# Optimization experiments

Measured on AMD Instinct MI355X. Metric: run time of the kernel, lower is better.

## Reference

```python
import jax, jax.numpy as jnp
import numpy as np

NEG_SLOPE = 0.2
EPS = 1e-16  # PyG softmax eps


def gat_layer(x, edge_index, W_lin, b_lin, W_attn, b_attn):
    # GATConv: add self loops, x = lin(x), per-edge attention, segment softmax over
    # target nodes (edge_index[1]), scatter-add of x_j * alpha.
    N = x.shape[0]
    loops = jnp.arange(N, dtype=edge_index.dtype)
    src = jnp.concatenate([edge_index[0], loops])  # j (source / neighbor)
    dst = jnp.concatenate([edge_index[1], loops])  # i (target)
    x = x @ W_lin.T + b_lin                        # [N, D]
    D = x.shape[1]
    xi = x[dst]                                    # [E, D]
    xj = x[src]                                    # [E, D]
    # attn(cat(x_i, x_j)) split to avoid materializing the [E, 2D] concat
    Wi, Wj = W_attn[:, :D], W_attn[:, D:]
    alpha = xi @ Wi.T + xj @ Wj.T + b_attn         # [E, D]
    alpha = jax.nn.leaky_relu(alpha, NEG_SLOPE)
    # numerically stable segment softmax grouped by dst (per output channel)
    m = jax.ops.segment_max(alpha, dst, num_segments=N)
    alpha = jnp.exp(alpha - m[dst])
    denom = jax.ops.segment_sum(alpha, dst, num_segments=N)
    alpha = alpha / (denom[dst] + EPS)
    return jax.ops.segment_sum(xj * alpha, dst, num_segments=N)


def setup_inputs() -> dict:
    key = jax.random.key(0)
    ks = jax.random.split(key, 22)
    B, L, NN, E = 64, 50, 500, 256000
    EMB, D = 128, 128
    N = B * NN
    w = lambda k, shape: jax.random.normal(k, shape, jnp.float32) * 0.05
    return {
        "x": jax.random.normal(ks[0], (N, EMB), jnp.float32),
        "edge_index_0": jax.random.randint(ks[1], (2, E), 0, N, jnp.int32),
        "edge_index_1": jax.random.randint(ks[2], (2, E), 0, N, jnp.int32),
        "state_": jax.random.normal(ks[3], (B, D), jnp.float32),
        "input_": jax.random.normal(ks[4], (B, L, EMB), jnp.float32),
        "W_in": w(ks[5], (D, EMB)),
        "W_z": w(ks[6], (D, 2 * D)),
        "W_r": w(ks[7], (D, 2 * D)),
        "W_h": w(ks[8], (D, 2 * D)),
        "g0_Wlin": w(ks[9], (D, EMB)),
        "g0_blin": w(ks[10], (D,)),
        "g0_Wattn": w(ks[11], (D, 2 * D)),
        "g0_battn": w(ks[12], (D,)),
        "g1_Wlin": w(ks[13], (D, D)),
        "g1_blin": w(ks[14], (D,)),
        "g1_Wattn": w(ks[15], (D, 2 * D)),
        "g1_battn": w(ks[16], (D,)),
        "Wp": w(ks[17], (1, D)),
        "bp": w(ks[18], (1,)),
        "Ws": w(ks[19], (1, D)),
        "bs": w(ks[20], (1,)),
    }


def reference(x, edge_index_0, edge_index_1, state_, input_,
              W_in, W_z, W_r, W_h,
              g0_Wlin, g0_blin, g0_Wattn, g0_battn,
              g1_Wlin, g1_blin, g1_Wattn, g1_battn,
              Wp, bp, Ws, bs):
    B, D = state_.shape
    n_nodes = x.shape[0] // B
    # GRU-style gate on global state
    inp = jnp.mean(input_ @ W_in.T, axis=1)                 # [B, D]
    zi = jnp.concatenate([state_, inp], axis=-1)            # [B, 2D]
    z = jax.nn.sigmoid(zi @ W_z.T)
    r = jax.nn.sigmoid(zi @ W_r.T)
    h = jnp.tanh(jnp.concatenate([r * state_, inp], -1) @ W_h.T)
    h = (1 - z) * state_ + z * h                            # [B, D]
    # two GAT layers
    g0 = gat_layer(x, edge_index_0, g0_Wlin, g0_blin, g0_Wattn, g0_battn)
    g1 = gat_layer(g0, edge_index_1, g1_Wlin, g1_blin, g1_Wattn, g1_battn)
    xg = g1.reshape(B, n_nodes, D) * h[:, None, :]          # broadcast gate
    prob = (xg @ Wp.T + bp).reshape(B, n_nodes)
    sisr = jax.nn.sigmoid((xg @ Ws.T + bs).reshape(B, n_nodes))
    prob = jax.nn.softmax(prob[:, 1:], axis=-1)             # drop depot node 0
    return prob, sisr, h
```

## Files before the change

### kernel.cpp

```cpp
#include <hip/hip_runtime.h>
#include <math.h>

#define CAP  32
#define CAPB 4096
#define PART_CHUNK 4096

typedef __attribute__((ext_vector_type(8))) short bfrag;
typedef __attribute__((ext_vector_type(4))) float ffrag;
typedef __attribute__((ext_vector_type(2))) float f2v;

__device__ __forceinline__ float sigmoidf_(float x){ return 1.f/(1.f+__expf(-x)); }

__device__ __forceinline__ unsigned short f2bf(float f){
    unsigned u = __float_as_uint(f);
    u += 0x7fffu + ((u >> 16) & 1u);
    return (unsigned short)(u >> 16);
}
__device__ __forceinline__ float bf2f(unsigned u){
    return __uint_as_float((u & 0xffffu) << 16);
}

__global__ __launch_bounds__(256) void prep_kernel(
    const int* __restrict__ ei0, const int* __restrict__ ei1,
    int* __restrict__ binCnt, unsigned* __restrict__ bins, int E, int nA, int nb,
    const float* __restrict__ state_, const float* __restrict__ input_,
    const float* __restrict__ W_in, const float* __restrict__ W_z,
    const float* __restrict__ W_r, const float* __restrict__ W_h,
    float* __restrict__ h_out, int L,
    const float* __restrict__ Wlin0, const float* __restrict__ Wattn0,
    const float* __restrict__ blin0, const float* __restrict__ battn0,
    const float* __restrict__ Wlin1, const float* __restrict__ Wattn1,
    const float* __restrict__ blin1, const float* __restrict__ battn1,
    unsigned short* __restrict__ wc, float* __restrict__ bc, int B)
{
    int blk = blockIdx.x;
    if (blk < 2 * nA) {
        __shared__ int lcnt[128];
        __shared__ int gbase[128];
        int g = (blk >= nA) ? 1 : 0;
        const int* ei = g ? ei1 : ei0;
        int base = (blk - g * nA) * PART_CHUNK;
        int tid = threadIdx.x;
        for (int t = tid; t < nb; t += 256) lcnt[t] = 0;
        __syncthreads();
        int lpos[16], binv[16]; unsigned wrd[16];
        #pragma unroll
        for (int i = 0; i < 16; ++i) {
            int e = base + i * 256 + tid;
            if (e < E) {
                int d = ei[E + e];
                int s = ei[e];
                int b = d >> 8;
                binv[i] = b;
                wrd[i]  = ((unsigned)(d & 255) << 24) | (unsigned)s;
                lpos[i] = atomicAdd(&lcnt[b], 1);
            } else binv[i] = -1;
        }
        __syncthreads();
        if (tid < nb) gbase[tid] = atomicAdd(&binCnt[g * nb + tid], lcnt[tid]);
        __syncthreads();
        #pragma unroll
        for (int i = 0; i < 16; ++i) {
            if (binv[i] >= 0) {
                int pos = gbase[binv[i]] + lpos[i];
                if (pos < CAPB) bins[(size_t)(g * nb + binv[i]) * CAPB + pos] = wrd[i];
            }
        }
    } else if (blk < 2 * nA + B) {
        __shared__ float mu[128];
        __shared__ float zi[256];
        __shared__ float zi2[256];
        int b = blk - 2 * nA;
        int tid = threadIdx.x;
        float st = 0.f, inp = 0.f, z = 0.f, r = 0.f;
        if (tid < 128) {
            float s = 0.f;
            const float* ip = input_ + (size_t)b * L * 128 + tid;
            for (int l = 0; l < L; ++l) s += ip[(size_t)l * 128];
            mu[tid] = s / (float)L;
        }
        __syncthreads();
        if (tid < 128) {
            const float* wr = W_in + (size_t)tid * 128;
            for (int k = 0; k < 128; ++k) inp += mu[k] * wr[k];
            st = state_[b * 128 + tid];
            zi[tid] = st; zi[128 + tid] = inp;
        }
        __syncthreads();
        if (tid < 128) {
            float az = 0.f, ar = 0.f;
            const float* wz = W_z + (size_t)tid * 256;
            const float* wrr = W_r + (size_t)tid * 256;
            for (int k = 0; k < 256; ++k) { float v = zi[k]; az += v * wz[k]; ar += v * wrr[k]; }
            z = sigmoidf_(az); r = sigmoidf_(ar);
            zi2[tid] = r * st; zi2[128 + tid] = inp;
        }
        __syncthreads();
        if (tid < 128) {
            float ah = 0.f;
            const float* wh = W_h + (size_t)tid * 256;
            for (int k = 0; k < 256; ++k) ah += zi2[k] * wh[k];
            float hc = tanhf(ah);
            h_out[b * 128 + tid] = (1.f - z) * st + z * hc;
        }
    } else {
        int idx = (blk - 2 * nA - B) * 256 + threadIdx.x;
        if (idx < 2 * 384 * 128) {
            int layer = idx / 49152;
            int t = idx - layer * 49152;
            int n = t >> 7, k = t & 127;
            const float* Wlin  = layer ? Wlin1  : Wlin0;
            const float* Wattn = layer ? Wattn1 : Wattn0;
            float v;
            if (n < 128) {
                v = Wlin[n * 128 + k];
            } else {
                int rr = (n < 256) ? (n - 128) : (n - 256);
                int off = (n < 256) ? 0 : 128;
                float s = 0.f;
                for (int d = 0; d < 128; ++d) s += Wattn[rr * 256 + off + d] * Wlin[d * 128 + k];
                v = s;
            }
            wc[idx] = f2bf(v);
        } else if (idx < 2 * 384 * 128 + 768) {
            int bi = idx - 2 * 384 * 128;
            int layer = bi / 384;
            int n = bi - layer * 384;
            const float* blin  = layer ? blin1  : blin0;
            const float* Wattn = layer ? Wattn1 : Wattn0;
            const float* battn = layer ? battn1 : battn0;
            float v;
            if (n < 128) v = blin[n];
            else {
                int rr = (n < 256) ? (n - 128) : (n - 256);
                int off = (n < 256) ? 0 : 128;
                float s = 0.f;
                for (int d = 0; d < 128; ++d) s += Wattn[rr * 256 + off + d] * blin[d];
                v = (n < 256) ? (s + battn[rr]) : s;
            }
            bc[bi] = v;
        }
    }
}

__global__ __launch_bounds__(256) void gemm384(const short* __restrict__ Xb, const float* __restrict__ Xf,
                                               const short* __restrict__ Wc, const float* __restrict__ bc,
                                               unsigned short* __restrict__ aib, unsigned short* __restrict__ pair,
                                               const unsigned* __restrict__ bins, const int* __restrict__ binCnt,
                                               int* __restrict__ cnt, unsigned short* __restrict__ esrc,
                                               int N, int nb, int gemmBlks)
{
    if ((int)blockIdx.x >= gemmBlks) {
        __shared__ int cl[256];
        __shared__ __align__(16) unsigned short el[256 * CAP];
        int p = blockIdx.x - gemmBlks;
        int g = (p >= nb) ? 1 : 0;
        int bin = p - g * nb;
        int tid = threadIdx.x;
        cl[tid] = 0;
        __syncthreads();
        int m = binCnt[g * nb + bin]; if (m > CAPB) m = CAPB;
        const unsigned* bp_ = bins + (size_t)(g * nb + bin) * CAPB;
        for (int i = tid; i < m; i += 256) {
            unsigned w = bp_[i];
            int dl = (int)(w >> 24);
            int pp = atomicAdd(&cl[dl], 1);
            if (pp < CAP) el[dl * CAP + pp] = (unsigned short)w;
        }
        __syncthreads();
        int nodeBase = bin * 256;
        int* cg = cnt + (size_t)g * N;
        if (nodeBase + tid < N) cg[nodeBase + tid] = cl[tid];
        uint4* eo = (uint4*)(esrc + ((size_t)g * N + nodeBase) * CAP);
        const uint4* es = (const uint4*)el;
        #pragma unroll
        for (int k = 0; k < 4; ++k) eo[k * 256 + tid] = es[k * 256 + tid];
        return;
    }
    __shared__ __align__(16) short wlds[384 * 40];
    int tid = threadIdx.x;
    int lane = tid & 63, wave = tid >> 6;
    int quad = lane >> 4, l16 = lane & 15;
    int mrow = blockIdx.x * 64 + wave * 16 + l16;

    bfrag av[4];
    if (Xf) {
        #pragma unroll
        for (int kk = 0; kk < 4; ++kk) {
            const float* xfp = Xf + (size_t)mrow * 128 + quad * 8 + kk * 32;
            float4 a0 = *(const float4*)(xfp);
            float4 a1 = *(const float4*)(xfp + 4);
            av[kk] = (bfrag){ (short)f2bf(a0.x), (short)f2bf(a0.y), (short)f2bf(a0.z), (short)f2bf(a0.w),
                              (short)f2bf(a1.x), (short)f2bf(a1.y), (short)f2bf(a1.z), (short)f2bf(a1.w) };
        }
    } else {
        #pragma unroll
        for (int kk = 0; kk < 4; ++kk)
            av[kk] = *(const bfrag*)(Xb + (size_t)mrow * 128 + quad * 8 + kk * 32);
    }

    ffrag acc[24];
    #pragma unroll
    for (int t = 0; t < 24; ++t) acc[t] = (ffrag){0.f, 0.f, 0.f, 0.f};

    #pragma unroll
    for (int kk = 0; kk < 4; ++kk) {
        __syncthreads();
        #pragma unroll
        for (int it = 0; it < 6; ++it) {
            int slot = it * 256 + tid;
            int row = slot >> 2, ch = slot & 3;
            *(bfrag*)&wlds[row * 40 + ch * 8] = *(const bfrag*)(Wc + (size_t)row * 128 + kk * 32 + ch * 8);
        }
        __syncthreads();
        #pragma unroll
        for (int t = 0; t < 24; ++t) {
            bfrag bv = *(const bfrag*)&wlds[(t * 16 + l16) * 40 + quad * 8];
            acc[t] = __builtin_amdgcn_mfma_f32_16x16x32_bf16(av[kk], bv, acc[t], 0, 0, 0);
        }
    }
    int rbase = blockIdx.x * 64 + wave * 16 + quad * 4;
    #pragma unroll
    for (int t = 0; t < 8; ++t) {
        int c = t * 16 + l16;
        float by = bc[c], bi = bc[128 + c], bj = bc[256 + c];
        #pragma unroll
        for (int r = 0; r < 4; ++r) {
            size_t off = (size_t)(rbase + r) * 128 + c;
            float yv  = acc[t][r]      + by;
            float aiv = acc[8 + t][r]  + bi;
            float ajv = acc[16 + t][r] + bj;
            aib[off] = f2bf(aiv);
            int w = __builtin_amdgcn_cvt_pk_fp8_f32(yv, ajv, 0, false);
            pair[off] = (unsigned short)w;
        }
    }
}

__global__ void aggregate_kernel(const unsigned short* __restrict__ aib, const unsigned* __restrict__ pair,
                                 const int* __restrict__ cnt, const unsigned short* __restrict__ esrc,
                                 unsigned* __restrict__ gb_out,
                                 const float* __restrict__ h, const float* __restrict__ Wp, const float* __restrict__ bp,
                                 const float* __restrict__ Ws, const float* __restrict__ bs,
                                 float* __restrict__ pbuf, float* __restrict__ sisr_out,
                                 int N, int NN, int fuse_score)
{
    int node = blockIdx.x * (blockDim.x >> 6) + (threadIdx.x >> 6);
    if (node >= N) return;
    int lane = threadIdx.x & 63;
    int c = 2 * lane;
    unsigned ain2 = *(const unsigned*)(aib + ((size_t)node << 7) + c);
    float ain0 = bf2f(ain2), ain1 = bf2f(ain2 >> 16);
    int deg = cnt[node]; if (deg > CAP) deg = CAP;
    const unsigned short* ep = esrc + (size_t)node * CAP;
    int myidx = (lane < deg) ? (int)ep[lane] : 0;

    float w0 = 0.f, w1 = 0.f, o0 = 0.f, o1 = 0.f;
    #define PROC(q) { \
        f2v lo = __builtin_amdgcn_cvt_pk_f32_fp8((int)(q), false); \
        f2v hi = __builtin_amdgcn_cvt_pk_f32_fp8((int)(q), true); \
        float a0 = ain0 + lo.y; \
        float a1 = ain1 + hi.y; \
        a0 = (a0 > 0.f) ? a0 : 0.2f * a0; \
        a1 = (a1 > 0.f) ? a1 : 0.2f * a1; \
        float e0 = __expf(a0), e1 = __expf(a1); \
        w0 += e0; w1 += e1; \
        o0 += e0 * lo.x; o1 += e1 * hi.x; }

    unsigned qs = pair[((size_t)node << 6) + lane];
    PROC(qs)

    int j = 0;
    for (; j + 8 <= deg; j += 8) {
        int s0 = __shfl(myidx, j),     s1 = __shfl(myidx, j + 1);
        int s2 = __shfl(myidx, j + 2), s3 = __shfl(myidx, j + 3);
        int s4 = __shfl(myidx, j + 4), s5 = __shfl(myidx, j + 5);
        int s6 = __shfl(myidx, j + 6), s7 = __shfl(myidx, j + 7);
        unsigned q0 = pair[((size_t)s0 << 6) + lane];
        unsigned q1 = pair[((size_t)s1 << 6) + lane];
        unsigned q2 = pair[((size_t)s2 << 6) + lane];
        unsigned q3 = pair[((size_t)s3 << 6) + lane];
        unsigned q4 = pair[((size_t)s4 << 6) + lane];
        unsigned q5 = pair[((size_t)s5 << 6) + lane];
        unsigned q6 = pair[((size_t)s6 << 6) + lane];
        unsigned q7 = pair[((size_t)s7 << 6) + lane];
        PROC(q0) PROC(q1) PROC(q2) PROC(q3) PROC(q4) PROC(q5) PROC(q6) PROC(q7)
    }
    if (j + 4 <= deg) {
        int s0 = __shfl(myidx, j),     s1 = __shfl(myidx, j + 1);
        int s2 = __shfl(myidx, j + 2), s3 = __shfl(myidx, j + 3);
        unsigned q0 = pair[((size_t)s0 << 6) + lane];
        unsigned q1 = pair[((size_t)s1 << 6) + lane];
        unsigned q2 = pair[((size_t)s2 << 6) + lane];
        unsigned q3 = pair[((size_t)s3 << 6) + lane];
        PROC(q0) PROC(q1) PROC(q2) PROC(q3)
        j += 4;
    }
    for (; j < deg; ++j) {
        int s0 = __shfl(myidx, j);
        unsigned q0 = pair[((size_t)s0 << 6) + lane];
        PROC(q0)
    }
    #undef PROC

    float g0 = o0 / (w0 + 1e-16f), g1 = o1 / (w1 + 1e-16f);
    if (!fuse_score) {
        gb_out[(size_t)node * 64 + lane] = (unsigned)f2bf(g0) | ((unsigned)f2bf(g1) << 16);
    } else {
        int b = node / NN;
        float xg0 = g0 * h[b * 128 + c], xg1 = g1 * h[b * 128 + c + 1];
        float pp = xg0 * Wp[c] + xg1 * Wp[c + 1];
        float ss = xg0 * Ws[c] + xg1 * Ws[c + 1];
        #pragma unroll
        for (int o = 32; o > 0; o >>= 1) { pp += __shfl_xor(pp, o); ss += __shfl_xor(ss, o); }
        if (lane == 0) {
            pbuf[node] = pp + bp[0];
            sisr_out[node] = sigmoidf_(ss + bs[0]);
        }
    }
}

__global__ void softmax_kernel(const float* __restrict__ pbuf, float* __restrict__ prob_out, int NN){
    int b = blockIdx.x, tid = threadIdx.x;
    __shared__ float sdata[512];
    bool valid = (tid >= 1 && tid < NN);
    float v = valid ? pbuf[b * NN + tid] : -INFINITY;
    sdata[tid] = v; __syncthreads();
    for (int o = 256; o > 0; o >>= 1) { if (tid < o) sdata[tid] = fmaxf(sdata[tid], sdata[tid + o]); __syncthreads(); }
    float m = sdata[0]; __syncthreads();
    float e = valid ? __expf(v - m) : 0.f;
    sdata[tid] = e; __syncthreads();
    for (int o = 256; o > 0; o >>= 1) { if (tid < o) sdata[tid] += sdata[tid + o]; __syncthreads(); }
    float ssum = sdata[0];
    if (valid) prob_out[(size_t)b * (NN - 1) + tid - 1] = e / ssum;
}

extern "C" void kernel_launch(void* const* d_in, const int* in_sizes, int n_in,
                              void* d_out, int out_size, void* d_ws, size_t ws_size,
                              hipStream_t stream)
{
    const float* x       = (const float*)d_in[0];
    const int*   ei0     = (const int*)d_in[1];
    const int*   ei1     = (const int*)d_in[2];
    const float* state_  = (const float*)d_in[3];
    const float* input_  = (const float*)d_in[4];
    const float* W_in    = (const float*)d_in[5];
    const float* W_z     = (const float*)d_in[6];
    const float* W_r     = (const float*)d_in[7];
    const float* W_h     = (const float*)d_in[8];
    const float* g0_Wlin = (const float*)d_in[9];
    const float* g0_blin = (const float*)d_in[10];
    const float* g0_Wattn= (const float*)d_in[11];
    const float* g0_battn= (const float*)d_in[12];
    const float* g1_Wlin = (const float*)d_in[13];
    const float* g1_blin = (const float*)d_in[14];
    const float* g1_Wattn= (const float*)d_in[15];
    const float* g1_battn= (const float*)d_in[16];
    const float* Wp      = (const float*)d_in[17];
    const float* bp      = (const float*)d_in[18];
    const float* Ws      = (const float*)d_in[19];
    const float* bs      = (const float*)d_in[20];

    const int N  = in_sizes[0] / 128;
    const int E  = in_sizes[1] / 2;
    const int B  = in_sizes[3] / 128;
    const int L  = in_sizes[4] / (B * 128);
    const int NN = N / B;
    const int nb = N >> 8;

    float* out      = (float*)d_out;
    float* prob_out = out;
    float* sisr_out = out + (size_t)B * (NN - 1);
    float* h_out    = sisr_out + (size_t)B * NN;

    unsigned short* aib = (unsigned short*)d_ws;
    unsigned* gbb  = (unsigned*)(aib + (size_t)N * 128);
    unsigned short* pair = (unsigned short*)(gbb + (size_t)N * 64);
    unsigned short* wc = pair + (size_t)N * 128;
    float* bc   = (float*)(wc + 2 * 384 * 128);
    float* pbuf = bc + 768;
    int* cnt0  = (int*)(pbuf + N);
    int* cnt1  = cnt0 + N;
    unsigned short* esrc0 = (unsigned short*)(cnt1 + N);
    unsigned short* esrc1 = esrc0 + (size_t)N * CAP;
    unsigned* bins = (unsigned*)(esrc1 + (size_t)N * CAP);
    int* binCnt = (int*)(bins + (size_t)2 * nb * CAPB);

    hipMemsetAsync(binCnt, 0, (size_t)2 * nb * sizeof(int), stream);

    const int nA = (E + PART_CHUNK - 1) / PART_CHUNK;
    prep_kernel<<<2 * nA + B + 387, 256, 0, stream>>>(
        ei0, ei1, binCnt, bins, E, nA, nb,
        state_, input_, W_in, W_z, W_r, W_h, h_out, L,
        g0_Wlin, g0_Wattn, g0_blin, g0_battn,
        g1_Wlin, g1_Wattn, g1_blin, g1_battn,
        wc, bc, B);

    const int gemmBlks = N / 64;

    gemm384<<<gemmBlks + 2 * nb, 256, 0, stream>>>(nullptr, x, (const short*)wc, bc, aib, pair,
                                                   bins, binCnt, cnt0, esrc0, N, nb, gemmBlks);

    aggregate_kernel<<<(N + 3) / 4, 256, 0, stream>>>(aib, (const unsigned*)pair, cnt0, esrc0, gbb,
                                                      nullptr, nullptr, nullptr, nullptr, nullptr,
                                                      nullptr, nullptr, N, NN, 0);

    gemm384<<<gemmBlks, 256, 0, stream>>>((const short*)gbb, nullptr, (const short*)(wc + 49152), bc + 384, aib, pair,
                                          nullptr, nullptr, nullptr, nullptr, N, nb, gemmBlks);

    aggregate_kernel<<<(N + 3) / 4, 256, 0, stream>>>(aib, (const unsigned*)pair, cnt1, esrc1, nullptr,
                                                      h_out, Wp, bp, Ws, bs,
                                                      pbuf, sisr_out, N, NN, 1);

    softmax_kernel<<<B, 512, 0, stream>>>(pbuf, prob_out, NN);
}
```

Measured before the change: 212.9 us.

## Fuse softmax into final aggregate via last-block counter; move GRU gate into second GEMM

The separate per-batch softmax kernel is removed. The final aggregate kernel now atomically counts finished nodes per batch, and the last wave to finish for a batch computes the softmax over its node scores. The GRU gate computation moves from the prep kernel into extra blocks of the second-layer GEMM launch, taking it off the prep kernel's critical path. This saves one kernel launch but adds agent-scope atomics per node and a serialized single-wave softmax tail per batch.

```diff
diff --git a/kernel.cpp b/kernel.cpp
--- a/kernel.cpp
+++ b/kernel.cpp
@@ -23,15 +23,11 @@
 __global__ __launch_bounds__(256) void prep_kernel(
     const int* __restrict__ ei0, const int* __restrict__ ei1,
     int* __restrict__ binCnt, unsigned* __restrict__ bins, int E, int nA, int nb,
-    const float* __restrict__ state_, const float* __restrict__ input_,
-    const float* __restrict__ W_in, const float* __restrict__ W_z,
-    const float* __restrict__ W_r, const float* __restrict__ W_h,
-    float* __restrict__ h_out, int L,
     const float* __restrict__ Wlin0, const float* __restrict__ Wattn0,
     const float* __restrict__ blin0, const float* __restrict__ battn0,
     const float* __restrict__ Wlin1, const float* __restrict__ Wattn1,
     const float* __restrict__ blin1, const float* __restrict__ battn1,
-    unsigned short* __restrict__ wc, float* __restrict__ bc, int B)
+    unsigned short* __restrict__ wc, float* __restrict__ bc)
 {
     int blk = blockIdx.x;
     if (blk < 2 * nA) {
@@ -66,45 +62,8 @@
                 if (pos < CAPB) bins[(size_t)(g * nb + binv[i]) * CAPB + pos] = wrd[i];
             }
         }
-    } else if (blk < 2 * nA + B) {
-        __shared__ float mu[128];
-        __shared__ float zi[256];
-        __shared__ float zi2[256];
-        int b = blk - 2 * nA;
-        int tid = threadIdx.x;
-        float st = 0.f, inp = 0.f, z = 0.f, r = 0.f;
-        if (tid < 128) {
-            float s = 0.f;
-            const float* ip = input_ + (size_t)b * L * 128 + tid;
-            for (int l = 0; l < L; ++l) s += ip[(size_t)l * 128];
-            mu[tid] = s / (float)L;
-        }
-        __syncthreads();
-        if (tid < 128) {
-            const float* wr = W_in + (size_t)tid * 128;
-            for (int k = 0; k < 128; ++k) inp += mu[k] * wr[k];
-            st = state_[b * 128 + tid];
-            zi[tid] = st; zi[128 + tid] = inp;
-        }
-        __syncthreads();
-        if (tid < 128) {
-            float az = 0.f, ar = 0.f;
-            const float* wz = W_z + (size_t)tid * 256;
-            const float* wrr = W_r + (size_t)tid * 256;
-            for (int k = 0; k < 256; ++k) { float v = zi[k]; az += v * wz[k]; ar += v * wrr[k]; }
-            z = sigmoidf_(az); r = sigmoidf_(ar);
-            zi2[tid] = r * st; zi2[128 + tid] = inp;
-        }
-        __syncthreads();
-        if (tid < 128) {
-            float ah = 0.f;
-            const float* wh = W_h + (size_t)tid * 256;
-            for (int k = 0; k < 256; ++k) ah += zi2[k] * wh[k];
-            float hc = tanhf(ah);
-            h_out[b * 128 + tid] = (1.f - z) * st + z * hc;
-        }
     } else {
-        int idx = (blk - 2 * nA - B) * 256 + threadIdx.x;
+        int idx = (blk - 2 * nA) * 256 + threadIdx.x;
         if (idx < 2 * 384 * 128) {
             int layer = idx / 49152;
             int t = idx - layer * 49152;
@@ -148,33 +107,76 @@
                                                unsigned short* __restrict__ aib, unsigned short* __restrict__ pair,
                                                const unsigned* __restrict__ bins, const int* __restrict__ binCnt,
                                                int* __restrict__ cnt, unsigned short* __restrict__ esrc,
+                                               const float* __restrict__ state_, const float* __restrict__ input_,
+                                               const float* __restrict__ W_in, const float* __restrict__ W_z,
+                                               const float* __restrict__ W_r, const float* __restrict__ W_h,
+                                               float* __restrict__ h_out, int L,
                                                int N, int nb, int gemmBlks)
 {
     if ((int)blockIdx.x >= gemmBlks) {
-        __shared__ int cl[256];
-        __shared__ __align__(16) unsigned short el[256 * CAP];
         int p = blockIdx.x - gemmBlks;
-        int g = (p >= nb) ? 1 : 0;
-        int bin = p - g * nb;
-        int tid = threadIdx.x;
-        cl[tid] = 0;
-        __syncthreads();
-        int m = binCnt[g * nb + bin]; if (m > CAPB) m = CAPB;
-        const unsigned* bp_ = bins + (size_t)(g * nb + bin) * CAPB;
-        for (int i = tid; i < m; i += 256) {
-            unsigned w = bp_[i];
-            int dl = (int)(w >> 24);
-            int pp = atomicAdd(&cl[dl], 1);
-            if (pp < CAP) el[dl * CAP + pp] = (unsigned short)w;
-        }
-        __syncthreads();
-        int nodeBase = bin * 256;
-        int* cg = cnt + (size_t)g * N;
-        if (nodeBase + tid < N) cg[nodeBase + tid] = cl[tid];
-        uint4* eo = (uint4*)(esrc + ((size_t)g * N + nodeBase) * CAP);
-        const uint4* es = (const uint4*)el;
-        #pragma unroll
-        for (int k = 0; k < 4; ++k) eo[k * 256 + tid] = es[k * 256 + tid];
+        if (bins) {
+            __shared__ int cl[256];
+            __shared__ __align__(16) unsigned short el[256 * CAP];
+            int g = (p >= nb) ? 1 : 0;
+            int bin = p - g * nb;
+            int tid = threadIdx.x;
+            cl[tid] = 0;
+            __syncthreads();
+            int m = binCnt[g * nb + bin]; if (m > CAPB) m = CAPB;
+            const unsigned* bp_ = bins + (size_t)(g * nb + bin) * CAPB;
+            for (int i = tid; i < m; i += 256) {
+                unsigned w = bp_[i];
+                int dl = (int)(w >> 24);
+                int pp = atomicAdd(&cl[dl], 1);
+                if (pp < CAP) el[dl * CAP + pp] = (unsigned short)w;
+            }
+            __syncthreads();
+            int nodeBase = bin * 256;
+            int* cg = cnt + (size_t)g * N;
+            if (nodeBase + tid < N) cg[nodeBase + tid] = cl[tid];
+            uint4* eo = (uint4*)(esrc + ((size_t)g * N + nodeBase) * CAP);
+            const uint4* es = (const uint4*)el;
+            #pragma unroll
+            for (int k = 0; k < 4; ++k) eo[k * 256 + tid] = es[k * 256 + tid];
+        } else {
+            __shared__ float mu[128];
+            __shared__ float zi[256];
+            __shared__ float zi2[256];
+            int b = p;
+            int tid = threadIdx.x;
+            float st = 0.f, inp = 0.f, z = 0.f, r = 0.f;
+            if (tid < 128) {
+                float s = 0.f;
+                const float* ip = input_ + (size_t)b * L * 128 + tid;
+                for (int l = 0; l < L; ++l) s += ip[(size_t)l * 128];
+                mu[tid] = s / (float)L;
+            }
+            __syncthreads();
+            if (tid < 128) {
+                const float* wr = W_in + (size_t)tid * 128;
+                for (int k = 0; k < 128; ++k) inp += mu[k] * wr[k];
+                st = state_[b * 128 + tid];
+                zi[tid] = st; zi[128 + tid] = inp;
+            }
+            __syncthreads();
+            if (tid < 128) {
+                float az = 0.f, ar = 0.f;
+                const float* wz = W_z + (size_t)tid * 256;
+                const float* wrr = W_r + (size_t)tid * 256;
+                for (int k = 0; k < 256; ++k) { float v = zi[k]; az += v * wz[k]; ar += v * wrr[k]; }
+                z = sigmoidf_(az); r = sigmoidf_(ar);
+                zi2[tid] = r * st; zi2[128 + tid] = inp;
+            }
+            __syncthreads();
+            if (tid < 128) {
+                float ah = 0.f;
+                const float* wh = W_h + (size_t)tid * 256;
+                for (int k = 0; k < 256; ++k) ah += zi2[k] * wh[k];
+                float hc = tanhf(ah);
+                h_out[b * 128 + tid] = (1.f - z) * st + z * hc;
+            }
+        }
         return;
     }
     __shared__ __align__(16) short wlds[384 * 40];
@@ -243,6 +245,7 @@
                                  const float* __restrict__ h, const float* __restrict__ Wp, const float* __restrict__ bp,
                                  const float* __restrict__ Ws, const float* __restrict__ bs,
                                  float* __restrict__ pbuf, float* __restrict__ sisr_out,
+                                 float* __restrict__ prob_out, int* __restrict__ done,
                                  int N, int NN, int fuse_score)
 {
     int node = blockIdx.x * (blockDim.x >> 6) + (threadIdx.x >> 6);
@@ -313,26 +316,44 @@
         float ss = xg0 * Ws[c] + xg1 * Ws[c + 1];
         #pragma unroll
         for (int o = 32; o > 0; o >>= 1) { pp += __shfl_xor(pp, o); ss += __shfl_xor(ss, o); }
+        int last = 0;
         if (lane == 0) {
-            pbuf[node] = pp + bp[0];
+            __hip_atomic_store(&pbuf[node], pp + bp[0], __ATOMIC_RELAXED, __HIP_MEMORY_SCOPE_AGENT);
             sisr_out[node] = sigmoidf_(ss + bs[0]);
-        }
-    }
-}
-
-__global__ void softmax_kernel(const float* __restrict__ pbuf, float* __restrict__ prob_out, int NN){
-    int b = blockIdx.x, tid = threadIdx.x;
-    __shared__ float sdata[512];
-    bool valid = (tid >= 1 && tid < NN);
-    float v = valid ? pbuf[b * NN + tid] : -INFINITY;
-    sdata[tid] = v; __syncthreads();
-    for (int o = 256; o > 0; o >>= 1) { if (tid < o) sdata[tid] = fmaxf(sdata[tid], sdata[tid + o]); __syncthreads(); }
-    float m = sdata[0]; __syncthreads();
-    float e = valid ? __expf(v - m) : 0.f;
-    sdata[tid] = e; __syncthreads();
-    for (int o = 256; o > 0; o >>= 1) { if (tid < o) sdata[tid] += sdata[tid + o]; __syncthreads(); }
-    float ssum = sdata[0];
-    if (valid) prob_out[(size_t)b * (NN - 1) + tid - 1] = e / ssum;
+            int old = __hip_atomic_fetch_add(&done[b], 1, __ATOMIC_ACQ_REL, __HIP_MEMORY_SCOPE_AGENT);
+            last = (old == NN - 1);
+        }
+        last = __shfl(last, 0);
+        if (last) {
+            float v[8];
+            float m = -INFINITY;
+            #pragma unroll
+            for (int rr = 0; rr < 8; ++rr) {
+                int i = rr * 64 + lane;
+                v[rr] = (i >= 1 && i < NN)
+                    ? __hip_atomic_load(&pbuf[(size_t)b * NN + i], __ATOMIC_RELAXED, __HIP_MEMORY_SCOPE_AGENT)
+                    : -INFINITY;
+                m = fmaxf(m, v[rr]);
+            }
+            #pragma unroll
+            for (int o = 32; o > 0; o >>= 1) m = fmaxf(m, __shfl_xor(m, o));
+            float s = 0.f;
+            #pragma unroll
+            for (int rr = 0; rr < 8; ++rr) {
+                int i = rr * 64 + lane;
+                v[rr] = (i >= 1 && i < NN) ? __expf(v[rr] - m) : 0.f;
+                s += v[rr];
+            }
+            #pragma unroll
+            for (int o = 32; o > 0; o >>= 1) s += __shfl_xor(s, o);
+            float inv = 1.f / s;
+            #pragma unroll
+            for (int rr = 0; rr < 8; ++rr) {
+                int i = rr * 64 + lane;
+                if (i >= 1 && i < NN) prob_out[(size_t)b * (NN - 1) + i - 1] = v[rr] * inv;
+            }
+        }
+    }
 }
 
 extern "C" void kernel_launch(void* const* d_in, const int* in_sizes, int n_in,
@@ -385,32 +406,34 @@
     unsigned short* esrc1 = esrc0 + (size_t)N * CAP;
     unsigned* bins = (unsigned*)(esrc1 + (size_t)N * CAP);
     int* binCnt = (int*)(bins + (size_t)2 * nb * CAPB);
-
-    hipMemsetAsync(binCnt, 0, (size_t)2 * nb * sizeof(int), stream);
+    int* done   = binCnt + 2 * nb;
+
+    hipMemsetAsync(binCnt, 0, (size_t)(2 * nb + B) * sizeof(int), stream);
 
     const int nA = (E + PART_CHUNK - 1) / PART_CHUNK;
-    prep_kernel<<<2 * nA + B + 387, 256, 0, stream>>>(
+    prep_kernel<<<2 * nA + 387, 256, 0, stream>>>(
         ei0, ei1, binCnt, bins, E, nA, nb,
-        state_, input_, W_in, W_z, W_r, W_h, h_out, L,
         g0_Wlin, g0_Wattn, g0_blin, g0_battn,
         g1_Wlin, g1_Wattn, g1_blin, g1_battn,
-        wc, bc, B);
+        wc, bc);
 
     const int gemmBlks = N / 64;
 
     gemm384<<<gemmBlks + 2 * nb, 256, 0, stream>>>(nullptr, x, (const short*)wc, bc, aib, pair,
-                                                   bins, binCnt, cnt0, esrc0, N, nb, gemmBlks);
+                                                   bins, binCnt, cnt0, esrc0,
+                                                   nullptr, nullptr, nullptr, nullptr, nullptr, nullptr,
+                                                   nullptr, L, N, nb, gemmBlks);
 
     aggregate_kernel<<<(N + 3) / 4, 256, 0, stream>>>(aib, (const unsigned*)pair, cnt0, esrc0, gbb,
                                                       nullptr, nullptr, nullptr, nullptr, nullptr,
-                                                      nullptr, nullptr, N, NN, 0);
-
-    gemm384<<<gemmBlks, 256, 0, stream>>>((const short*)gbb, nullptr, (const short*)(wc + 49152), bc + 384, aib, pair,
-                                          nullptr, nullptr, nullptr, nullptr, N, nb, gemmBlks);
+                                                      nullptr, nullptr, nullptr, nullptr, N, NN, 0);
+
+    gemm384<<<gemmBlks + B, 256, 0, stream>>>((const short*)gbb, nullptr, (const short*)(wc + 49152), bc + 384, aib, pair,
+                                              nullptr, nullptr, nullptr, nullptr,
+                                              state_, input_, W_in, W_z, W_r, W_h,
+                                              h_out, L, N, nb, gemmBlks);
 
     aggregate_kernel<<<(N + 3) / 4, 256, 0, stream>>>(aib, (const unsigned*)pair, cnt1, esrc1, nullptr,
                                                       h_out, Wp, bp, Ws, bs,
-                                                      pbuf, sisr_out, N, NN, 1);
-
-    softmax_kernel<<<B, 512, 0, stream>>>(pbuf, prob_out, NN);
-}
+                                                      pbuf, sisr_out, prob_out, done, N, NN, 1);
+}
```

After: 804.1 us. 278% more time.
